# Performance work log

Measured on AMD Instinct MI355X. Metric: run time of the kernel, lower is better.

## Reference

```python
import jax, jax.numpy as jnp
import numpy as np

B = 2_000_000      # minibatch of tuple ids
N_DF = 4_000_000   # rows in combined df (rows of mat)
R = 8              # number of rules
M = 1_000_000      # rows in each rule's df (size of rule_output buffer)
NAN_FRAC = 0.25    # fraction of (tuple, rule) slots that are NaN (rule doesn't contribute)


def setup_inputs() -> dict:
    key = jax.random.key(0)
    k_x, k_idx, k_nan, k_tab, k_alpha, k_slack = jax.random.split(key, 6)
    x = jax.random.randint(k_x, (B,), 0, N_DF, dtype=jnp.int32)
    # mat: float matrix of per-rule row indices into each rule's df, NaN where rule absent
    idx = jax.random.randint(k_idx, (N_DF, R), 0, M).astype(jnp.float32)
    nan_mask = jax.random.uniform(k_nan, (N_DF, R)) < NAN_FRAC
    mat = jnp.where(nan_mask, jnp.float32(jnp.nan), idx)
    # each rule modeled as a learned prediction per tuple index + a scalar slack
    rule_tables = jax.random.normal(k_tab, (R, M), dtype=jnp.float32)
    alpha_logits = jax.random.normal(k_alpha, (R, 1), dtype=jnp.float32)
    slack_params = jax.random.normal(k_slack, (R,), dtype=jnp.float32)
    return {"x": x, "mat": mat, "rule_tables": rule_tables,
            "alpha_logits": alpha_logits, "slack_params": slack_params}


def reference(x, mat, rule_tables, alpha_logits, slack_params):
    # tmp = mat[x, :] : [B, R] float indices with NaN for missing contributions
    tmp = mat[x]
    valid = ~jnp.isnan(tmp)                      # my_where valid mask
    idx = jnp.where(valid, tmp, 0.0).astype(jnp.int32)   # safe gather indices
    # rule_output[idx] = rules[i](unique(idx)) followed by my_where gather
    # collapses to a direct per-rule gather, zero where NaN. [B, R]
    gathered = rule_tables[jnp.arange(R)[None, :], idx]  # [B, R]
    activations = jnp.where(valid, gathered, 0.0)
    # alpha[choice]: learned attention over rules (predicates1(R, 1)) -> [B, 1]
    w = jax.nn.softmax(alpha_logits, axis=0)     # [R, 1]
    ret = activations @ w                        # [B, 1]
    slacks = jnp.sum(slack_params)               # accumulated local_slacks
    return (ret, slacks)
```

## Files before the change

### kernel.cpp

```cpp
#include <hip/hip_runtime.h>
#include <math.h>

#define RR 8
#define MM 1000000

typedef float     f32x4 __attribute__((ext_vector_type(4)));
typedef int       i32x4 __attribute__((ext_vector_type(4)));
typedef int       i32x2 __attribute__((ext_vector_type(2)));
typedef _Float16  f16x4 __attribute__((ext_vector_type(4)));

__global__ void prep_kernel(const float* __restrict__ alpha_logits,
                            const float* __restrict__ slack_params,
                            float* __restrict__ w_out,
                            float* __restrict__ slack_out) {
    if (threadIdx.x == 0 && blockIdx.x == 0) {
        float a[RR];
        float m = -INFINITY;
        #pragma unroll
        for (int r = 0; r < RR; ++r) { a[r] = alpha_logits[r]; m = fmaxf(m, a[r]); }
        float s = 0.f;
        #pragma unroll
        for (int r = 0; r < RR; ++r) { a[r] = expf(a[r] - m); s += a[r]; }
        float inv = 1.0f / s;
        float ss = 0.f;
        #pragma unroll
        for (int r = 0; r < RR; ++r) { w_out[r] = a[r] * inv; ss += slack_params[r]; }
        *slack_out = ss;
    }
}

__global__ __launch_bounds__(256) void gather_mat_kernel(
    const int* __restrict__ x,
    const float* __restrict__ mat,
    int* __restrict__ tmp, int B) {
    int half = B >> 1;
    int t = blockIdx.x * 256 + threadIdx.x;
    if (t >= half) return;
    i32x2 xx = __builtin_nontemporal_load(reinterpret_cast<const i32x2*>(x) + t);
    const f32x4* mp = reinterpret_cast<const f32x4*>(mat);
    long long r0 = (long long)xx.x, r1 = (long long)xx.y;
    f32x4 a0 = mp[r0 * 2];
    f32x4 a1 = mp[r0 * 2 + 1];
    f32x4 b0 = mp[r1 * 2];
    f32x4 b1 = mp[r1 * 2 + 1];
    float va[RR] = {a0.x, a0.y, a0.z, a0.w, a1.x, a1.y, a1.z, a1.w};
    float vb[RR] = {b0.x, b0.y, b0.z, b0.w, b1.x, b1.y, b1.z, b1.w};
    #pragma unroll
    for (int r = 0; r < RR; ++r) {
        i32x2 o;
        float u = va[r], v = vb[r];
        o.x = (u != u) ? -1 : (int)u;
        o.y = (v != v) ? -1 : (int)v;
        __builtin_nontemporal_store(o, reinterpret_cast<i32x2*>(tmp + (size_t)r * B) + t);
    }
}

__global__ __launch_bounds__(256) void rule_gather_kernel(
    const int* __restrict__ tmp,
    const float* __restrict__ rule_tables,
    _Float16* __restrict__ partial, int B) {
    int rule  = blockIdx.x & 7;
    int chunk = blockIdx.x >> 3;
    int Nv = B >> 2;
    int t = chunk * 256 + threadIdx.x;
    if (t >= Nv) return;
    const i32x4* tp4 = reinterpret_cast<const i32x4*>(tmp + (size_t)rule * B);
    const float* tab = rule_tables + (size_t)rule * MM;
    f16x4*       pp4 = reinterpret_cast<f16x4*>(partial + (size_t)rule * B);

    i32x4 iv = __builtin_nontemporal_load(tp4 + t);
    float g0 = tab[iv.x >= 0 ? iv.x : 0];
    float g1 = tab[iv.y >= 0 ? iv.y : 0];
    float g2 = tab[iv.z >= 0 ? iv.z : 0];
    float g3 = tab[iv.w >= 0 ? iv.w : 0];
    f16x4 o;
    o.x = (_Float16)(iv.x >= 0 ? g0 : 0.f);
    o.y = (_Float16)(iv.y >= 0 ? g1 : 0.f);
    o.z = (_Float16)(iv.z >= 0 ? g2 : 0.f);
    o.w = (_Float16)(iv.w >= 0 ? g3 : 0.f);
    __builtin_nontemporal_store(o, pp4 + t);
}

__global__ __launch_bounds__(256) void reduce_kernel(
    const _Float16* __restrict__ partial,
    const float* __restrict__ w_vec,
    float* __restrict__ out, int B) {
    int Nv = B >> 2;
    int t = blockIdx.x * 256 + threadIdx.x;
    if (t >= Nv) return;
    f32x4 acc = {0.f, 0.f, 0.f, 0.f};
    #pragma unroll
    for (int r = 0; r < RR; ++r) {
        f16x4 v = __builtin_nontemporal_load(
            reinterpret_cast<const f16x4*>(partial + (size_t)r * B) + t);
        float wr = w_vec[r];
        acc.x += wr * (float)v.x;
        acc.y += wr * (float)v.y;
        acc.z += wr * (float)v.z;
        acc.w += wr * (float)v.w;
    }
    __builtin_nontemporal_store(acc, reinterpret_cast<f32x4*>(out) + t);
}

__global__ __launch_bounds__(256) void meta_pred_kernel(
    const int* __restrict__ x,
    const float* __restrict__ mat,
    const float* __restrict__ rule_tables,
    const float* __restrict__ w_vec,
    float* __restrict__ out, int B) {
    int b = blockIdx.x * blockDim.x + threadIdx.x;
    if (b >= B) return;
    f32x4 wlo = *reinterpret_cast<const f32x4*>(w_vec);
    f32x4 whi = *reinterpret_cast<const f32x4*>(w_vec + 4);
    float w[RR] = {wlo.x, wlo.y, wlo.z, wlo.w, whi.x, whi.y, whi.z, whi.w};
    long long row = (long long)x[b];
    const f32x4* mp = reinterpret_cast<const f32x4*>(mat + row * RR);
    f32x4 v0 = mp[0];
    f32x4 v1 = mp[1];
    float vals[RR] = {v0.x, v0.y, v0.z, v0.w, v1.x, v1.y, v1.z, v1.w};
    bool valid[RR]; int idx[RR];
    #pragma unroll
    for (int r = 0; r < RR; ++r) {
        float v = vals[r];
        valid[r] = !(v != v);
        idx[r] = valid[r] ? (int)v : 0;
    }
    float g[RR];
    #pragma unroll
    for (int r = 0; r < RR; ++r) g[r] = rule_tables[(size_t)r * MM + (size_t)idx[r]];
    float acc = 0.f;
    #pragma unroll
    for (int r = 0; r < RR; ++r) acc += valid[r] ? g[r] * w[r] : 0.f;
    out[b] = acc;
}

extern "C" void kernel_launch(void* const* d_in, const int* in_sizes, int n_in,
                              void* d_out, int out_size, void* d_ws, size_t ws_size,
                              hipStream_t stream) {
    const int*   x            = (const int*)d_in[0];
    const float* mat          = (const float*)d_in[1];
    const float* rule_tables  = (const float*)d_in[2];
    const float* alpha_logits = (const float*)d_in[3];
    const float* slack_params = (const float*)d_in[4];

    const int B = in_sizes[0];
    float* out   = (float*)d_out;
    float* w_vec = (float*)d_ws;

    prep_kernel<<<1, 64, 0, stream>>>(alpha_logits, slack_params, w_vec, out + B);

    size_t tmp_bytes     = (size_t)RR * (size_t)B * sizeof(int);
    size_t partial_bytes = (size_t)RR * (size_t)B * sizeof(_Float16);
    size_t needed = 256 + tmp_bytes + partial_bytes;
    bool divisible = (B % 16) == 0;

    if (ws_size >= needed && divisible) {
        int*      tmp     = (int*)((char*)d_ws + 256);
        _Float16* partial = (_Float16*)((char*)d_ws + 256 + tmp_bytes);

        int half  = B >> 1;
        int grid1 = (half + 255) / 256;
        gather_mat_kernel<<<grid1, 256, 0, stream>>>(x, mat, tmp, B);

        int Nv = B >> 2;
        int chunks2 = (Nv + 255) / 256;
        rule_gather_kernel<<<chunks2 * RR, 256, 0, stream>>>(tmp, rule_tables, partial, B);

        int grid3 = (Nv + 255) / 256;
        reduce_kernel<<<grid3, 256, 0, stream>>>(partial, w_vec, out, B);
    } else {
        int grid = (B + 255) / 256;
        meta_pred_kernel<<<grid, 256, 0, stream>>>(x, mat, rule_tables, w_vec, out, B);
    }
}
```

Before: 129.2 us.

## Pack per-rule gather indices into 20-bit lo/hi split and widen reduce loads

The intermediate index buffer goes from 32-bit ints to 20-bit values, stored as a 16-bit low half packed in pairs into uint32 plus a 4-bit nibble array, with 0xFFFFF marking NaN. This cuts the bytes written by the mat gather kernel and read by the rule gather kernel. The reduce kernel also loads 8 fp16 partials per thread and writes two float4s. The cost is extra bit manipulation, byte-sized stores in the first kernel and 2-byte loads in the second, and indices that are only correct while below 2^20.

```diff
diff --git a/kernel.cpp b/kernel.cpp
--- a/kernel.cpp
+++ b/kernel.cpp
@@ -3,11 +3,12 @@
 
 #define RR 8
 #define MM 1000000
+#define NANI 0xFFFFF
 
 typedef float     f32x4 __attribute__((ext_vector_type(4)));
 typedef int       i32x4 __attribute__((ext_vector_type(4)));
 typedef int       i32x2 __attribute__((ext_vector_type(2)));
-typedef _Float16  f16x4 __attribute__((ext_vector_type(4)));
+typedef _Float16  f16x8 __attribute__((ext_vector_type(8)));
 
 __global__ void prep_kernel(const float* __restrict__ alpha_logits,
                             const float* __restrict__ slack_params,
@@ -32,7 +33,9 @@
 __global__ __launch_bounds__(256) void gather_mat_kernel(
     const int* __restrict__ x,
     const float* __restrict__ mat,
-    int* __restrict__ tmp, int B) {
+    unsigned int* __restrict__ lo,
+    unsigned char* __restrict__ hi,
+    int B) {
     int half = B >> 1;
     int t = blockIdx.x * 256 + threadIdx.x;
     if (t >= half) return;
@@ -45,18 +48,22 @@
     f32x4 b1 = mp[r1 * 2 + 1];
     float va[RR] = {a0.x, a0.y, a0.z, a0.w, a1.x, a1.y, a1.z, a1.w};
     float vb[RR] = {b0.x, b0.y, b0.z, b0.w, b1.x, b1.y, b1.z, b1.w};
+    size_t halfB = (size_t)half;
     #pragma unroll
     for (int r = 0; r < RR; ++r) {
-        i32x2 o;
         float u = va[r], v = vb[r];
-        o.x = (u != u) ? -1 : (int)u;
-        o.y = (v != v) ? -1 : (int)v;
-        __builtin_nontemporal_store(o, reinterpret_cast<i32x2*>(tmp + (size_t)r * B) + t);
+        unsigned ia = (u != u) ? NANI : (unsigned)(int)u;
+        unsigned ib = (v != v) ? NANI : (unsigned)(int)v;
+        unsigned lod = (ia & 0xFFFFu) | ((ib & 0xFFFFu) << 16);
+        unsigned char hb = (unsigned char)((ia >> 16) | ((ib >> 16) << 4));
+        __builtin_nontemporal_store(lod, lo + (size_t)r * halfB + t);
+        __builtin_nontemporal_store(hb, hi + (size_t)r * halfB + t);
     }
 }
 
 __global__ __launch_bounds__(256) void rule_gather_kernel(
-    const int* __restrict__ tmp,
+    const unsigned int* __restrict__ lo,
+    const unsigned char* __restrict__ hi,
     const float* __restrict__ rule_tables,
     _Float16* __restrict__ partial, int B) {
     int rule  = blockIdx.x & 7;
@@ -64,42 +71,60 @@
     int Nv = B >> 2;
     int t = chunk * 256 + threadIdx.x;
     if (t >= Nv) return;
-    const i32x4* tp4 = reinterpret_cast<const i32x4*>(tmp + (size_t)rule * B);
+    size_t halfB = (size_t)(B >> 1);
+    const unsigned int*  lp = lo + (size_t)rule * halfB;
+    const unsigned char* hp = hi + (size_t)rule * halfB;
     const float* tab = rule_tables + (size_t)rule * MM;
-    f16x4*       pp4 = reinterpret_cast<f16x4*>(partial + (size_t)rule * B);
-
-    i32x4 iv = __builtin_nontemporal_load(tp4 + t);
-    float g0 = tab[iv.x >= 0 ? iv.x : 0];
-    float g1 = tab[iv.y >= 0 ? iv.y : 0];
-    float g2 = tab[iv.z >= 0 ? iv.z : 0];
-    float g3 = tab[iv.w >= 0 ? iv.w : 0];
-    f16x4 o;
-    o.x = (_Float16)(iv.x >= 0 ? g0 : 0.f);
-    o.y = (_Float16)(iv.y >= 0 ? g1 : 0.f);
-    o.z = (_Float16)(iv.z >= 0 ? g2 : 0.f);
-    o.w = (_Float16)(iv.w >= 0 ? g3 : 0.f);
-    __builtin_nontemporal_store(o, pp4 + t);
+
+    i32x2 l2 = __builtin_nontemporal_load(reinterpret_cast<const i32x2*>(lp) + t);
+    unsigned short hh = *reinterpret_cast<const unsigned short*>(hp + 2 * (size_t)t);
+
+    unsigned i0 = ((unsigned)l2.x & 0xFFFFu) | ((unsigned)(hh       & 0xF) << 16);
+    unsigned i1 = ((unsigned)l2.x >> 16)     | ((unsigned)((hh>>4)  & 0xF) << 16);
+    unsigned i2 = ((unsigned)l2.y & 0xFFFFu) | ((unsigned)((hh>>8)  & 0xF) << 16);
+    unsigned i3 = ((unsigned)l2.y >> 16)     | ((unsigned)((hh>>12) & 0xF) << 16);
+
+    float g0 = tab[i0 != NANI ? i0 : 0u];
+    float g1 = tab[i1 != NANI ? i1 : 0u];
+    float g2 = tab[i2 != NANI ? i2 : 0u];
+    float g3 = tab[i3 != NANI ? i3 : 0u];
+
+    _Float16 o0 = (_Float16)(i0 != NANI ? g0 : 0.f);
+    _Float16 o1 = (_Float16)(i1 != NANI ? g1 : 0.f);
+    _Float16 o2 = (_Float16)(i2 != NANI ? g2 : 0.f);
+    _Float16 o3 = (_Float16)(i3 != NANI ? g3 : 0.f);
+    union { _Float16 h[4]; i32x2 d; } pk;
+    pk.h[0] = o0; pk.h[1] = o1; pk.h[2] = o2; pk.h[3] = o3;
+    __builtin_nontemporal_store(pk.d,
+        reinterpret_cast<i32x2*>(partial + (size_t)rule * B) + t);
 }
 
 __global__ __launch_bounds__(256) void reduce_kernel(
     const _Float16* __restrict__ partial,
     const float* __restrict__ w_vec,
     float* __restrict__ out, int B) {
-    int Nv = B >> 2;
+    int N8 = B >> 3;
     int t = blockIdx.x * 256 + threadIdx.x;
-    if (t >= Nv) return;
-    f32x4 acc = {0.f, 0.f, 0.f, 0.f};
+    if (t >= N8) return;
+    f32x4 accL = {0.f, 0.f, 0.f, 0.f};
+    f32x4 accH = {0.f, 0.f, 0.f, 0.f};
     #pragma unroll
     for (int r = 0; r < RR; ++r) {
-        f16x4 v = __builtin_nontemporal_load(
-            reinterpret_cast<const f16x4*>(partial + (size_t)r * B) + t);
+        f16x8 v = __builtin_nontemporal_load(
+            reinterpret_cast<const f16x8*>(partial + (size_t)r * B) + t);
         float wr = w_vec[r];
-        acc.x += wr * (float)v.x;
-        acc.y += wr * (float)v.y;
-        acc.z += wr * (float)v.z;
-        acc.w += wr * (float)v.w;
-    }
-    __builtin_nontemporal_store(acc, reinterpret_cast<f32x4*>(out) + t);
+        accL.x += wr * (float)v.s0;
+        accL.y += wr * (float)v.s1;
+        accL.z += wr * (float)v.s2;
+        accL.w += wr * (float)v.s3;
+        accH.x += wr * (float)v.s4;
+        accH.y += wr * (float)v.s5;
+        accH.z += wr * (float)v.s6;
+        accH.w += wr * (float)v.s7;
+    }
+    f32x4* op = reinterpret_cast<f32x4*>(out);
+    __builtin_nontemporal_store(accL, op + 2 * (size_t)t);
+    __builtin_nontemporal_store(accH, op + 2 * (size_t)t + 1);
 }
 
 __global__ __launch_bounds__(256) void meta_pred_kernel(
@@ -149,24 +174,28 @@
 
     prep_kernel<<<1, 64, 0, stream>>>(alpha_logits, slack_params, w_vec, out + B);
 
-    size_t tmp_bytes     = (size_t)RR * (size_t)B * sizeof(int);
+    size_t halfB = (size_t)B >> 1;
+    size_t lo_bytes      = (size_t)RR * halfB * sizeof(unsigned int);
+    size_t hi_bytes      = (size_t)RR * halfB * sizeof(unsigned char);
     size_t partial_bytes = (size_t)RR * (size_t)B * sizeof(_Float16);
-    size_t needed = 256 + tmp_bytes + partial_bytes;
+    size_t needed = 256 + lo_bytes + hi_bytes + partial_bytes;
     bool divisible = (B % 16) == 0;
 
     if (ws_size >= needed && divisible) {
-        int*      tmp     = (int*)((char*)d_ws + 256);
-        _Float16* partial = (_Float16*)((char*)d_ws + 256 + tmp_bytes);
+        unsigned int*  lo      = (unsigned int*)((char*)d_ws + 256);
+        unsigned char* hi      = (unsigned char*)((char*)d_ws + 256 + lo_bytes);
+        _Float16*      partial = (_Float16*)((char*)d_ws + 256 + lo_bytes + hi_bytes);
 
         int half  = B >> 1;
         int grid1 = (half + 255) / 256;
-        gather_mat_kernel<<<grid1, 256, 0, stream>>>(x, mat, tmp, B);
+        gather_mat_kernel<<<grid1, 256, 0, stream>>>(x, mat, lo, hi, B);
 
         int Nv = B >> 2;
         int chunks2 = (Nv + 255) / 256;
-        rule_gather_kernel<<<chunks2 * RR, 256, 0, stream>>>(tmp, rule_tables, partial, B);
-
-        int grid3 = (Nv + 255) / 256;
+        rule_gather_kernel<<<chunks2 * RR, 256, 0, stream>>>(lo, hi, rule_tables, partial, B);
+
+        int N8 = B >> 3;
+        int grid3 = (N8 + 255) / 256;
         reduce_kernel<<<grid3, 256, 0, stream>>>(partial, w_vec, out, B);
     } else {
         int grid = (B + 255) / 256;
```

Result: faster. 125.6 us (-2.8%).
